# Performance work log

Measured on AMD Instinct MI355X. Metric: run time of the kernel, lower is better.

Reference implementation:

```python
import jax, jax.numpy as jnp
import numpy as np

HIDDEN = 1024
N_HEADS = 16
HEAD_DIM = HIDDEN // N_HEADS
WINDOW = 256
HALF_W = WINDOW // 2  # 128
GLOBAL_TOKENS = (0,)


def setup_inputs() -> dict:
    key = jax.random.key(0)
    ks = jax.random.split(key, 5)
    B, S = 1, 4096
    scale = 0.02
    return {
        "x": jax.random.normal(ks[0], (B, S, HIDDEN), dtype=jnp.float32),
        "Wq": jax.random.normal(ks[1], (HIDDEN, HIDDEN), dtype=jnp.float32) * scale,
        "Wk": jax.random.normal(ks[2], (HIDDEN, HIDDEN), dtype=jnp.float32) * scale,
        "Wv": jax.random.normal(ks[3], (HIDDEN, HIDDEN), dtype=jnp.float32) * scale,
        "Wo": jax.random.normal(ks[4], (HIDDEN, HIDDEN), dtype=jnp.float32) * scale,
    }


def _longformer_mask(seq_len: int) -> jnp.ndarray:
    # sliding window |i-j| <= half_w, plus full rows/cols for global tokens
    idx = jnp.arange(seq_len)
    mask = jnp.abs(idx[:, None] - idx[None, :]) <= HALF_W
    for g in GLOBAL_TOKENS:
        if 0 <= g < seq_len:
            mask = mask.at[g, :].set(True)
            mask = mask.at[:, g].set(True)
    return mask  # [S, S] bool


def reference(x, Wq, Wk, Wv, Wo):
    B, S, H = x.shape
    scale = HEAD_DIM ** -0.5
    # nn.Linear(bias=False): y = x @ W.T ; split heads -> [B, nH, S, hd]
    def proj(W):
        return jnp.einsum('bsh,oh->bso', x, W).reshape(B, S, N_HEADS, HEAD_DIM).transpose(0, 2, 1, 3)
    q, k, v = proj(Wq), proj(Wk), proj(Wv)
    scores = jnp.einsum('bnsd,bntd->bnst', q, k) * scale  # [B, nH, S, S]
    mask = _longformer_mask(S)
    scores = jnp.where(mask[None, None], scores, jnp.float32(-jnp.inf))
    attn = jax.nn.softmax(scores, axis=-1)
    out = jnp.einsum('bnst,bntd->bnsd', attn, v)  # [B, nH, S, hd]
    out = out.transpose(0, 2, 1, 3).reshape(B, S, H)
    return jnp.einsum('bsh,oh->bso', out, Wo)
```

## Files before the change

### kernel.cpp

```cpp
#include <hip/hip_runtime.h>
#include <hip/hip_bf16.h>
#include <stdint.h>

#define S_LEN 4096
#define HID   1024
#define NH    16
#define HD    64
#define HWIN  128

typedef __bf16 bf16x8 __attribute__((ext_vector_type(8)));
typedef float  f32x4  __attribute__((ext_vector_type(4)));
typedef unsigned short u16x8 __attribute__((ext_vector_type(8)));

typedef const __attribute__((address_space(1))) unsigned int* gas_ptr;
typedef __attribute__((address_space(3))) unsigned int* las_ptr;

__device__ __forceinline__ float bf2f(unsigned short u) {
  union { float f; uint32_t i; } w; w.i = ((uint32_t)u) << 16; return w.f;
}
__device__ __forceinline__ unsigned short f2bf(float f) {
  union { float f; uint32_t i; } w; w.f = f;
  uint32_t r = (w.i + 0x7FFFu + ((w.i >> 16) & 1u)) >> 16;
  return (unsigned short)r;
}

__device__ __forceinline__ void gld_lds16(const void* g, void* l) {
  __builtin_amdgcn_global_load_lds((gas_ptr)g, (las_ptr)l, 16, 0, 0);
}

__global__ __launch_bounds__(256) void convert_all(
    const float* __restrict__ x,
    const float* __restrict__ wq, const float* __restrict__ wk,
    const float* __restrict__ wv, const float* __restrict__ wo,
    unsigned short* __restrict__ xb,
    unsigned short* __restrict__ wqb, unsigned short* __restrict__ wkb,
    unsigned short* __restrict__ wvb, unsigned short* __restrict__ wob) {
  const int XF4 = (S_LEN * HID) / 4;
  const int WF4 = (HID * HID) / 4;
  int i = blockIdx.x * 256 + threadIdx.x;
#pragma unroll
  for (int it = 0; it < 4; it++, i += 524288) {
    const float* in; unsigned short* out; int off;
    if (i < XF4) { in = x; out = xb; off = i; }
    else {
      int j = i - XF4;
      int w = j >> 18;
      off = j & (WF4 - 1);
      switch (w) {
        case 0:  in = wq; out = wqb; break;
        case 1:  in = wk; out = wkb; break;
        case 2:  in = wv; out = wvb; break;
        default: in = wo; out = wob; break;
      }
    }
    float4 v = reinterpret_cast<const float4*>(in)[off];
    ushort4 o;
    o.x = f2bf(v.x); o.y = f2bf(v.y); o.z = f2bf(v.z); o.w = f2bf(v.w);
    reinterpret_cast<ushort4*>(out)[off] = o;
  }
}

__device__ __forceinline__ void gemm_body(const unsigned short* __restrict__ A,
                                          const unsigned short* __restrict__ B,
                                          unsigned short* __restrict__ Cb,
                                          float* __restrict__ Cf, int mode) {
  __shared__ __align__(16) unsigned short SM[2 * 128 * 64];
  unsigned short* As = SM;
  unsigned short* Bs = SM + 128 * 64;
  constexpr int K = HID;
  const int tid  = threadIdx.x;
  const int lane = tid & 63;
  const int wave = tid >> 6;
  const int wm = wave >> 1, wn = wave & 1;
  const int m0 = blockIdx.x * 128;
  const int n0 = blockIdx.y * 128;
  const int cl = lane & 15, g = lane >> 4;

  f32x4 acc[4][4];
#pragma unroll
  for (int i = 0; i < 4; i++)
#pragma unroll
    for (int j = 0; j < 4; j++) acc[i][j] = f32x4{0.f, 0.f, 0.f, 0.f};

  const unsigned short* Ap[4];
  const unsigned short* Bp[4];
  int ldso[4];
#pragma unroll
  for (int u = 0; u < 4; u++) {
    int s = tid + u * 256;
    int row = s >> 3, c16 = s & 7;
    int sc = ((c16 ^ (row & 7)) << 3);
    Ap[u] = A + (size_t)(m0 + row) * K + sc;
    Bp[u] = B + (size_t)(n0 + row) * K + sc;
    ldso[u] = s * 8;
  }

  for (int k0 = 0; k0 < K; k0 += 64) {
#pragma unroll
    for (int u = 0; u < 4; u++) {
      gld_lds16(Ap[u] + k0, &As[ldso[u]]);
      gld_lds16(Bp[u] + k0, &Bs[ldso[u]]);
    }
    __syncthreads();
#pragma unroll
    for (int kk = 0; kk < 2; kk++) {
      bf16x8 a[4], b[4];
#pragma unroll
      for (int mi = 0; mi < 4; mi++) {
        int row = wm * 64 + mi * 16 + cl;
        int c16 = (kk * 4 + g) ^ (row & 7);
        a[mi] = *reinterpret_cast<const bf16x8*>(&As[row * 64 + c16 * 8]);
      }
#pragma unroll
      for (int ni = 0; ni < 4; ni++) {
        int row = wn * 64 + ni * 16 + cl;
        int c16 = (kk * 4 + g) ^ (row & 7);
        b[ni] = *reinterpret_cast<const bf16x8*>(&Bs[row * 64 + c16 * 8]);
      }
#pragma unroll
      for (int mi = 0; mi < 4; mi++)
#pragma unroll
        for (int ni = 0; ni < 4; ni++)
          acc[mi][ni] = __builtin_amdgcn_mfma_f32_16x16x32_bf16(a[mi], b[ni], acc[mi][ni], 0, 0, 0);
    }
    __syncthreads();
  }

  const int rl = g * 4;
  if (mode == 1) {
#pragma unroll
    for (int mi = 0; mi < 4; mi++)
#pragma unroll
      for (int ni = 0; ni < 4; ni++) {
        int c = wn * 64 + ni * 16 + cl;
        int slot = (wm * 16 + mi * 4 + g) ^ ((c & 7) << 2);
        uint2 u;
        u.x = (uint32_t)f2bf(acc[mi][ni][0]) | ((uint32_t)f2bf(acc[mi][ni][1]) << 16);
        u.y = (uint32_t)f2bf(acc[mi][ni][2]) | ((uint32_t)f2bf(acc[mi][ni][3]) << 16);
        *reinterpret_cast<uint2*>(&SM[c * 128 + slot * 4]) = u;
      }
    __syncthreads();
    const int rgrp = tid & 15;
#pragma unroll
    for (int p = 0; p < 8; p++) {
      int c = p * 16 + (tid >> 4);
      int s0 = (2 * rgrp) ^ ((c & 7) << 2);
      int s1 = (2 * rgrp + 1) ^ ((c & 7) << 2);
      uint2 a2 = *reinterpret_cast<const uint2*>(&SM[c * 128 + s0 * 4]);
      uint2 b2 = *reinterpret_cast<const uint2*>(&SM[c * 128 + s1 * 4]);
      uint4 o{a2.x, a2.y, b2.x, b2.y};
      *reinterpret_cast<uint4*>(&Cb[(size_t)(n0 + c) * S_LEN + m0 + rgrp * 8]) = o;
    }
    return;
  }
#pragma unroll
  for (int mi = 0; mi < 4; mi++)
#pragma unroll
    for (int ni = 0; ni < 4; ni++)
#pragma unroll
      for (int i = 0; i < 4; i++) {
        int r = m0 + wm * 64 + mi * 16 + rl + i;
        int c = n0 + wn * 64 + ni * 16 + cl;
        float v = acc[mi][ni][i];
        if (mode == 2) Cf[(size_t)r * HID + c] = v;
        else           Cb[(size_t)r * HID + c] = f2bf(v);
      }
}

__global__ __launch_bounds__(256, 2) void gemm_qkv(
    const unsigned short* __restrict__ xb,
    const unsigned short* __restrict__ wqb, const unsigned short* __restrict__ wkb,
    const unsigned short* __restrict__ wvb,
    unsigned short* __restrict__ Qb, unsigned short* __restrict__ Kb,
    unsigned short* __restrict__ Vt) {
  const unsigned short* B = (blockIdx.z == 0) ? wqb : (blockIdx.z == 1) ? wkb : wvb;
  unsigned short* C       = (blockIdx.z == 0) ? Qb  : (blockIdx.z == 1) ? Kb  : Vt;
  int mode = (blockIdx.z == 2) ? 1 : 0;
  gemm_body(xb, B, C, nullptr, mode);
}

__global__ __launch_bounds__(256, 2) void gemm_proj(
    unsigned short* __restrict__ Ob, const unsigned short* __restrict__ wob,
    const float* __restrict__ mw, const float* __restrict__ lw,
    const float* __restrict__ ow, float* __restrict__ out) {
  if (blockIdx.x == 0) {
    const float LOG2E = 1.44269504f;
    for (int cc = threadIdx.x; cc < HID; cc += 256) {
      int h = cc >> 6, d = cc & 63;
      float m_g = -1e30f;
#pragma unroll
      for (int c = 0; c < 16; c++) m_g = fmaxf(m_g, mw[h * 16 + c]);
      float lsum = 0.f, osum = 0.f;
#pragma unroll
      for (int c = 0; c < 16; c++) {
        float w = exp2f((mw[h * 16 + c] - m_g) * LOG2E);
        lsum += lw[h * 16 + c] * w;
        osum += ow[(size_t)(h * 16 + c) * HD + d] * w;
      }
      Ob[cc] = f2bf(osum / lsum);
    }
    asm volatile("s_waitcnt vmcnt(0)" ::: "memory");
    __syncthreads();
  }
  gemm_body(Ob, wob, nullptr, out, 2);
}

__global__ __launch_bounds__(256) void attn_win(
    const unsigned short* __restrict__ Qb,
    const unsigned short* __restrict__ Kb,
    const unsigned short* __restrict__ Vt,
    unsigned short* __restrict__ Ob,
    float* __restrict__ mw, float* __restrict__ lw, float* __restrict__ ow) {
  const int tid  = threadIdx.x;
  const int lane = tid & 63;
  const int wave = tid >> 6;

  if (blockIdx.x >= 1024) {
    const int bid = blockIdx.x - 1024;
    const int c = bid & 15, h = bid >> 4;
    const int k = c * 256 + tid;
    __shared__ float qsh[HD];
    __shared__ float ps[256];
    __shared__ float redm[4], redl[4];
    __shared__ float red2[4][HD];
    const float LOG2E = 1.44269504f;

    if (tid < HD) qsh[tid] = bf2f(Qb[h * HD + tid]);
    __syncthreads();

    const unsigned short* kr = Kb + (size_t)k * HID + h * HD;
    float acc = 0.f;
#pragma unroll
    for (int v8 = 0; v8 < 8; v8++) {
      u16x8 kv = *reinterpret_cast<const u16x8*>(kr + v8 * 8);
#pragma unroll
      for (int j = 0; j < 8; j++) acc += qsh[v8 * 8 + j] * bf2f(kv[j]);
    }
    float s = acc * 0.125f;

    float m = s;
#pragma unroll
    for (int d = 1; d < 64; d <<= 1) m = fmaxf(m, __shfl_xor(m, d, 64));
    if (lane == 0) redm[wave] = m;
    __syncthreads();
    float m_c = fmaxf(fmaxf(redm[0], redm[1]), fmaxf(redm[2], redm[3]));

    float p = exp2f((s - m_c) * LOG2E);
    ps[tid] = p;
    float l = p;
#pragma unroll
    for (int d = 1; d < 64; d <<= 1) l += __shfl_xor(l, d, 64);
    if (lane == 0) redl[wave] = l;
    __syncthreads();
    float l_c = redl[0] + redl[1] + redl[2] + redl[3];

    const int d = tid & 63, grp = tid >> 6;
    const unsigned short* vrow = Vt + (size_t)(h * HD + d) * S_LEN + c * 256 + grp * 64;
    float a2 = 0.f;
#pragma unroll
    for (int v8 = 0; v8 < 8; v8++) {
      u16x8 vv = *reinterpret_cast<const u16x8*>(vrow + v8 * 8);
#pragma unroll
      for (int j = 0; j < 8; j++) a2 += ps[grp * 64 + v8 * 8 + j] * bf2f(vv[j]);
    }
    red2[grp][d] = a2;
    __syncthreads();
    if (tid < HD) {
      float o = red2[0][tid] + red2[1][tid] + red2[2][tid] + red2[3][tid];
      ow[(size_t)(h * 16 + c) * HD + tid] = o;
    }
    if (tid == 0) { mw[h * 16 + c] = m_c; lw[h * 16 + c] = l_c; }
    return;
  }

  __shared__ __align__(16) unsigned short Kl[2][64 * 64];
  __shared__ __align__(16) unsigned short Vl[2][64 * 64];
  __shared__ __align__(16) unsigned short Ps[4][16 * 64];
  const int L  = (blockIdx.x & 7) * 128 + (blockIdx.x >> 3);
  const int h  = L >> 6;
  const int q0 = (L & 63) * 64;
  const int qr   = q0 + wave * 16;
  const int cl = lane & 15, g = lane >> 4, rl = g * 4;
  const float SCL = 0.125f * 1.44269504f;

  int kw0 = q0 - 128; if (kw0 < 0) kw0 = 0;
  int kw1 = q0 + 192; if (kw1 > S_LEN) kw1 = S_LEN;
  const int nc = (kw1 - kw0) >> 6;

  const int s0 = tid, s1 = tid + 256;
  const int kr0 = s0 >> 3, kc0 = ((s0 & 7) ^ (kr0 & 7)) << 3;
  const int kr1 = s1 >> 3, kc1 = ((s1 & 7) ^ (kr1 & 7)) << 3;
  const unsigned short* Kbase = Kb + h * HD;
  const unsigned short* Vbase = Vt + (size_t)h * HD * S_LEN;

  auto stage = [&](int kb, int b) {
    gld_lds16(Kbase + (size_t)(kb + kr0) * HID + kc0, &Kl[b][s0 * 8]);
    gld_lds16(Kbase + (size_t)(kb + kr1) * HID + kc1, &Kl[b][s1 * 8]);
    gld_lds16(Vbase + (size_t)kr0 * S_LEN + kb + kc0, &Vl[b][s0 * 8]);
    gld_lds16(Vbase + (size_t)kr1 * S_LEN + kb + kc1, &Vl[b][s1 * 8]);
  };

  stage(kw0, 0);

  bf16x8 qf[2], k0f[2];
  {
    const unsigned short* qb = Qb + (size_t)(qr + cl) * HID + h * HD + g * 8;
    qf[0] = *reinterpret_cast<const bf16x8*>(qb);
    qf[1] = *reinterpret_cast<const bf16x8*>(qb + 32);
    const unsigned short* k0 = Kb + h * HD + g * 8;
    k0f[0] = *reinterpret_cast<const bf16x8*>(k0);
    k0f[1] = *reinterpret_cast<const bf16x8*>(k0 + 32);
  }
  float v0[4];
#pragma unroll
  for (int nt = 0; nt < 4; nt++)
    v0[nt] = bf2f(Vt[(size_t)(h * HD + nt * 16 + cl) * S_LEN]);

  float m_i[4] = {-1e30f, -1e30f, -1e30f, -1e30f};
  float l_i[4] = {0.f, 0.f, 0.f, 0.f};
  f32x4 oacc[4];
#pragma unroll
  for (int nt = 0; nt < 4; nt++) oacc[nt] = f32x4{0.f, 0.f, 0.f, 0.f};

  __syncthreads();

  for (int c = 0; c < nc; c++) {
    const int cur = c & 1;
    const int kb = kw0 + c * 64;
    if (c + 1 < nc) stage(kw0 + (c + 1) * 64, cur ^ 1);

    bf16x8 kf[4][2];
#pragma unroll
    for (int t = 0; t < 4; t++) {
      int R = t * 16 + cl;
      kf[t][0] = *reinterpret_cast<const bf16x8*>(&Kl[cur][R * 64 + ((g ^ (R & 7)) << 3)]);
      kf[t][1] = *reinterpret_cast<const bf16x8*>(&Kl[cur][R * 64 + (((g + 4) ^ (R & 7)) << 3)]);
    }
    f32x4 s4[4];
    __builtin_amdgcn_s_setprio(1);
#pragma unroll
    for (int t = 0; t < 4; t++) {
      s4[t] = f32x4{0.f, 0.f, 0.f, 0.f};
      s4[t] = __builtin_amdgcn_mfma_f32_16x16x32_bf16(qf[0], kf[t][0], s4[t], 0, 0, 0);
      s4[t] = __builtin_amdgcn_mfma_f32_16x16x32_bf16(qf[1], kf[t][1], s4[t], 0, 0, 0);
    }
    __builtin_amdgcn_s_setprio(0);

    float sv[4][4], tm[4];
    if (kb >= qr - 113 && kb <= qr + 65) {
#pragma unroll
      for (int i = 0; i < 4; i++) {
        tm[i] = -1e30f;
#pragma unroll
        for (int t = 0; t < 4; t++) {
          float v = s4[t][i] * SCL;
          sv[t][i] = v;
          tm[i] = fmaxf(tm[i], v);
        }
      }
    } else {
#pragma unroll
      for (int i = 0; i < 4; i++) {
        int row = qr + rl + i;
        tm[i] = -1e30f;
#pragma unroll
        for (int t = 0; t < 4; t++) {
          int col = kb + t * 16 + cl;
          int d = row - col;
          float v = (d <= HWIN && d >= -HWIN) ? s4[t][i] * SCL : -1e30f;
          sv[t][i] = v;
          tm[i] = fmaxf(tm[i], v);
        }
      }
    }
#pragma unroll
    for (int dd = 1; dd < 16; dd <<= 1)
#pragma unroll
      for (int i = 0; i < 4; i++) tm[i] = fmaxf(tm[i], __shfl_xor(tm[i], dd, 16));

    float p[4][4], ps[4];
#pragma unroll
    for (int i = 0; i < 4; i++) {
      float mnew = fmaxf(m_i[i], tm[i]);
      float fac  = exp2f(m_i[i] - mnew);
      m_i[i] = mnew;
      float sum = 0.f;
#pragma unroll
      for (int t = 0; t < 4; t++) { p[t][i] = exp2f(sv[t][i] - mnew); sum += p[t][i]; }
      ps[i] = sum;
      l_i[i] *= fac;
#pragma unroll
      for (int nt = 0; nt < 4; nt++) oacc[nt][i] *= fac;
    }
#pragma unroll
    for (int dd = 1; dd < 16; dd <<= 1)
#pragma unroll
      for (int i = 0; i < 4; i++) ps[i] += __shfl_xor(ps[i], dd, 16);
#pragma unroll
    for (int i = 0; i < 4; i++) l_i[i] += ps[i];

#pragma unroll
    for (int t = 0; t < 4; t++)
#pragma unroll
      for (int i = 0; i < 4; i++) {
        int row = rl + i;
        Ps[wave][row * 64 + ((t * 16 + cl) ^ ((row & 7) << 3))] = f2bf(p[t][i]);
      }
    bf16x8 pf[2];
    pf[0] = *reinterpret_cast<const bf16x8*>(&Ps[wave][cl * 64 + ((g * 8) ^ ((cl & 7) << 3))]);
    pf[1] = *reinterpret_cast<const bf16x8*>(&Ps[wave][cl * 64 + ((32 + g * 8) ^ ((cl & 7) << 3))]);

    __builtin_amdgcn_s_setprio(1);
#pragma unroll
    for (int nt = 0; nt < 4; nt++) {
      int row = nt * 16 + cl;
      bf16x8 vf0 = *reinterpret_cast<const bf16x8*>(&Vl[cur][row * 64 + ((g ^ (row & 7)) << 3)]);
      bf16x8 vf1 = *reinterpret_cast<const bf16x8*>(&Vl[cur][row * 64 + (((g + 4) ^ (row & 7)) << 3)]);
      oacc[nt] = __builtin_amdgcn_mfma_f32_16x16x32_bf16(pf[0], vf0, oacc[nt], 0, 0, 0);
      oacc[nt] = __builtin_amdgcn_mfma_f32_16x16x32_bf16(pf[1], vf1, oacc[nt], 0, 0, 0);
    }
    __builtin_amdgcn_s_setprio(0);

    __syncthreads();
  }

  float part = 0.f;
#pragma unroll
  for (int s = 0; s < 2; s++)
#pragma unroll
    for (int j = 0; j < 8; j++) part += (float)qf[s][j] * (float)k0f[s][j];
  part += __shfl_xor(part, 16);
  part += __shfl_xor(part, 32);
  float s0q = part * SCL;
#pragma unroll
  for (int i = 0; i < 4; i++) {
    float z0 = __shfl(s0q, rl + i, 16);
    int row = qr + rl + i;
    if (row > HWIN) {
      float mnew = fmaxf(m_i[i], z0);
      float fac  = exp2f(m_i[i] - mnew);
      float p0   = exp2f(z0 - mnew);
      l_i[i] = l_i[i] * fac + p0;
#pragma unroll
      for (int nt = 0; nt < 4; nt++)
        oacc[nt][i] = oacc[nt][i] * fac + p0 * v0[nt];
    }
  }

#pragma unroll
  for (int nt = 0; nt < 4; nt++)
#pragma unroll
    for (int i = 0; i < 4; i++)
      Ob[(size_t)(qr + rl + i) * HID + h * HD + nt * 16 + cl] = f2bf(oacc[nt][i] / l_i[i]);
}

extern "C" void kernel_launch(void* const* d_in, const int* in_sizes, int n_in,
                              void* d_out, int out_size, void* d_ws, size_t ws_size,
                              hipStream_t stream) {
  const float* x  = (const float*)d_in[0];
  const float* wq = (const float*)d_in[1];
  const float* wk = (const float*)d_in[2];
  const float* wv = (const float*)d_in[3];
  const float* wo = (const float*)d_in[4];
  float* out = (float*)d_out;
  char* ws = (char*)d_ws;
  const size_t MB = 1024ull * 1024ull;
  unsigned short* xb  = (unsigned short*)(ws + 0 * MB);
  unsigned short* wqb = (unsigned short*)(ws + 8 * MB);
  unsigned short* wkb = (unsigned short*)(ws + 10 * MB);
  unsigned short* wvb = (unsigned short*)(ws + 12 * MB);
  unsigned short* wob = (unsigned short*)(ws + 14 * MB);
  unsigned short* Qb  = (unsigned short*)(ws + 16 * MB);
  unsigned short* Kb  = (unsigned short*)(ws + 24 * MB);
  unsigned short* Vt  = (unsigned short*)(ws + 32 * MB);
  unsigned short* Ob  = (unsigned short*)(ws + 40 * MB);
  float* mw = (float*)(ws + 48 * MB);
  float* lw = (float*)(ws + 48 * MB + 4096);
  float* ow = (float*)(ws + 48 * MB + 8192);

  dim3 blk(256);
  convert_all<<<dim3(2048), blk, 0, stream>>>(
      x, wq, wk, wv, wo, xb, wqb, wkb, wvb, wob);
  gemm_qkv<<<dim3(S_LEN / 128, HID / 128, 3), blk, 0, stream>>>(
      xb, wqb, wkb, wvb, Qb, Kb, Vt);
  attn_win<<<dim3(1280), blk, 0, stream>>>(Qb, Kb, Vt, Ob, mw, lw, ow);
  gemm_proj<<<dim3(S_LEN / 128, HID / 128), blk, 0, stream>>>(
      Ob, wob, mw, lw, ow, out);
}
```

Before: 91.53 us.

## Triple-buffer GEMM K-loop with async LDS loads and single barrier

```diff
diff --git a/kernel.cpp b/kernel.cpp
--- a/kernel.cpp
+++ b/kernel.cpp
@@ -64,10 +64,9 @@
                                           const unsigned short* __restrict__ B,
                                           unsigned short* __restrict__ Cb,
                                           float* __restrict__ Cf, int mode) {
-  __shared__ __align__(16) unsigned short SM[2 * 128 * 64];
-  unsigned short* As = SM;
-  unsigned short* Bs = SM + 128 * 64;
+  __shared__ __align__(16) unsigned short SM[24576];
   constexpr int K = HID;
+  constexpr int NT = K / 32;
   const int tid  = threadIdx.x;
   const int lane = tid & 63;
   const int wave = tid >> 6;
@@ -82,48 +81,62 @@
 #pragma unroll
     for (int j = 0; j < 4; j++) acc[i][j] = f32x4{0.f, 0.f, 0.f, 0.f};
 
-  const unsigned short* Ap[4];
-  const unsigned short* Bp[4];
-  int ldso[4];
-#pragma unroll
-  for (int u = 0; u < 4; u++) {
-    int s = tid + u * 256;
-    int row = s >> 3, c16 = s & 7;
-    int sc = ((c16 ^ (row & 7)) << 3);
-    Ap[u] = A + (size_t)(m0 + row) * K + sc;
-    Bp[u] = B + (size_t)(n0 + row) * K + sc;
-    ldso[u] = s * 8;
-  }
-
-  for (int k0 = 0; k0 < K; k0 += 64) {
-#pragma unroll
-    for (int u = 0; u < 4; u++) {
-      gld_lds16(Ap[u] + k0, &As[ldso[u]]);
-      gld_lds16(Bp[u] + k0, &Bs[ldso[u]]);
-    }
-    __syncthreads();
-#pragma unroll
-    for (int kk = 0; kk < 2; kk++) {
-      bf16x8 a[4], b[4];
-#pragma unroll
-      for (int mi = 0; mi < 4; mi++) {
-        int row = wm * 64 + mi * 16 + cl;
-        int c16 = (kk * 4 + g) ^ (row & 7);
-        a[mi] = *reinterpret_cast<const bf16x8*>(&As[row * 64 + c16 * 8]);
-      }
-#pragma unroll
-      for (int ni = 0; ni < 4; ni++) {
-        int row = wn * 64 + ni * 16 + cl;
-        int c16 = (kk * 4 + g) ^ (row & 7);
-        b[ni] = *reinterpret_cast<const bf16x8*>(&Bs[row * 64 + c16 * 8]);
-      }
-#pragma unroll
-      for (int mi = 0; mi < 4; mi++)
-#pragma unroll
-        for (int ni = 0; ni < 4; ni++)
-          acc[mi][ni] = __builtin_amdgcn_mfma_f32_16x16x32_bf16(a[mi], b[ni], acc[mi][ni], 0, 0, 0);
-    }
-    __syncthreads();
+  const int s0 = tid, s1 = tid + 256;
+  const int r0 = s0 >> 2, c0 = ((s0 & 3) ^ ((r0 >> 1) & 3)) << 3;
+  const int r1 = s1 >> 2, c1 = ((s1 & 3) ^ ((r1 >> 1) & 3)) << 3;
+  const unsigned short* A0 = A + (size_t)(m0 + r0) * K + c0;
+  const unsigned short* A1 = A + (size_t)(m0 + r1) * K + c1;
+  const unsigned short* B0 = B + (size_t)(n0 + r0) * K + c0;
+  const unsigned short* B1 = B + (size_t)(n0 + r1) * K + c1;
+
+  auto stage = [&](int t, int b) {
+    const int k0 = t * 32;
+    gld_lds16(A0 + k0, &SM[b * 4096 + s0 * 8]);
+    gld_lds16(A1 + k0, &SM[b * 4096 + s1 * 8]);
+    gld_lds16(B0 + k0, &SM[12288 + b * 4096 + s0 * 8]);
+    gld_lds16(B1 + k0, &SM[12288 + b * 4096 + s1 * 8]);
+  };
+
+  stage(0, 0);
+  stage(1, 1);
+  asm volatile("s_waitcnt vmcnt(4)" ::: "memory");
+  __builtin_amdgcn_s_barrier();
+  __builtin_amdgcn_sched_barrier(0);
+
+  int cur = 0;
+  for (int t = 0; t < NT; ++t) {
+    int nn = cur + 2; if (nn >= 3) nn -= 3;
+    const bool more = (t + 2 < NT);
+    if (more) stage(t + 2, nn);
+
+    const unsigned short* Ac = &SM[cur * 4096];
+    const unsigned short* Bc = &SM[12288 + cur * 4096];
+    bf16x8 a[4], b[4];
+#pragma unroll
+    for (int mi = 0; mi < 4; mi++) {
+      int row = wm * 64 + mi * 16 + cl;
+      a[mi] = *reinterpret_cast<const bf16x8*>(
+          &Ac[row * 32 + ((g ^ ((row >> 1) & 3)) << 3)]);
+    }
+#pragma unroll
+    for (int ni = 0; ni < 4; ni++) {
+      int row = wn * 64 + ni * 16 + cl;
+      b[ni] = *reinterpret_cast<const bf16x8*>(
+          &Bc[row * 32 + ((g ^ ((row >> 1) & 3)) << 3)]);
+    }
+    __builtin_amdgcn_s_setprio(1);
+#pragma unroll
+    for (int mi = 0; mi < 4; mi++)
+#pragma unroll
+      for (int ni = 0; ni < 4; ni++)
+        acc[mi][ni] = __builtin_amdgcn_mfma_f32_16x16x32_bf16(a[mi], b[ni], acc[mi][ni], 0, 0, 0);
+    __builtin_amdgcn_s_setprio(0);
+
+    if (more) asm volatile("s_waitcnt vmcnt(4)" ::: "memory");
+    else      asm volatile("s_waitcnt vmcnt(0)" ::: "memory");
+    __builtin_amdgcn_s_barrier();
+    __builtin_amdgcn_sched_barrier(0);
+    cur = (cur == 2) ? 0 : cur + 1;
   }
 
   const int rl = g * 4;
@@ -144,10 +157,10 @@
 #pragma unroll
     for (int p = 0; p < 8; p++) {
       int c = p * 16 + (tid >> 4);
-      int s0 = (2 * rgrp) ^ ((c & 7) << 2);
-      int s1 = (2 * rgrp + 1) ^ ((c & 7) << 2);
-      uint2 a2 = *reinterpret_cast<const uint2*>(&SM[c * 128 + s0 * 4]);
-      uint2 b2 = *reinterpret_cast<const uint2*>(&SM[c * 128 + s1 * 4]);
+      int sa = (2 * rgrp) ^ ((c & 7) << 2);
+      int sb = (2 * rgrp + 1) ^ ((c & 7) << 2);
+      uint2 a2 = *reinterpret_cast<const uint2*>(&SM[c * 128 + sa * 4]);
+      uint2 b2 = *reinterpret_cast<const uint2*>(&SM[c * 128 + sb * 4]);
       uint4 o{a2.x, a2.y, b2.x, b2.y};
       *reinterpret_cast<uint4*>(&Cb[(size_t)(n0 + c) * S_LEN + m0 + rgrp * 8]) = o;
     }
```

Result: slower. 94.13 us (+2.8%).

## Process two 16-row query tiles per wave to reuse K/V chunks in attention

Applied to the files above, without the earlier changes.

```diff
diff --git a/kernel.cpp b/kernel.cpp
--- a/kernel.cpp
+++ b/kernel.cpp
@@ -144,10 +144,10 @@
 #pragma unroll
     for (int p = 0; p < 8; p++) {
       int c = p * 16 + (tid >> 4);
-      int s0 = (2 * rgrp) ^ ((c & 7) << 2);
-      int s1 = (2 * rgrp + 1) ^ ((c & 7) << 2);
-      uint2 a2 = *reinterpret_cast<const uint2*>(&SM[c * 128 + s0 * 4]);
-      uint2 b2 = *reinterpret_cast<const uint2*>(&SM[c * 128 + s1 * 4]);
+      int sa = (2 * rgrp) ^ ((c & 7) << 2);
+      int sb = (2 * rgrp + 1) ^ ((c & 7) << 2);
+      uint2 a2 = *reinterpret_cast<const uint2*>(&SM[c * 128 + sa * 4]);
+      uint2 b2 = *reinterpret_cast<const uint2*>(&SM[c * 128 + sb * 4]);
       uint4 o{a2.x, a2.y, b2.x, b2.y};
       *reinterpret_cast<uint4*>(&Cb[(size_t)(n0 + c) * S_LEN + m0 + rgrp * 8]) = o;
     }
@@ -215,8 +215,8 @@
   const int lane = tid & 63;
   const int wave = tid >> 6;
 
-  if (blockIdx.x >= 1024) {
-    const int bid = blockIdx.x - 1024;
+  if (blockIdx.x >= 512) {
+    const int bid = blockIdx.x - 512;
     const int c = bid & 15, h = bid >> 4;
     const int k = c * 256 + tid;
     __shared__ float qsh[HD];
@@ -276,15 +276,15 @@
   __shared__ __align__(16) unsigned short Kl[2][64 * 64];
   __shared__ __align__(16) unsigned short Vl[2][64 * 64];
   __shared__ __align__(16) unsigned short Ps[4][16 * 64];
-  const int L  = (blockIdx.x & 7) * 128 + (blockIdx.x >> 3);
-  const int h  = L >> 6;
-  const int q0 = (L & 63) * 64;
-  const int qr   = q0 + wave * 16;
+  const int L  = (blockIdx.x & 7) * 64 + (blockIdx.x >> 3);
+  const int h  = L >> 5;
+  const int q0 = (L & 31) * 128;
+  const int qr0 = q0 + wave * 32;
   const int cl = lane & 15, g = lane >> 4, rl = g * 4;
   const float SCL = 0.125f * 1.44269504f;
 
   int kw0 = q0 - 128; if (kw0 < 0) kw0 = 0;
-  int kw1 = q0 + 192; if (kw1 > S_LEN) kw1 = S_LEN;
+  int kw1 = q0 + 256; if (kw1 > S_LEN) kw1 = S_LEN;
   const int nc = (kw1 - kw0) >> 6;
 
   const int s0 = tid, s1 = tid + 256;
@@ -302,11 +302,14 @@
 
   stage(kw0, 0);
 
-  bf16x8 qf[2], k0f[2];
+  bf16x8 qf[2][2], k0f[2];
   {
-    const unsigned short* qb = Qb + (size_t)(qr + cl) * HID + h * HD + g * 8;
-    qf[0] = *reinterpret_cast<const bf16x8*>(qb);
-    qf[1] = *reinterpret_cast<const bf16x8*>(qb + 32);
+#pragma unroll
+    for (int qt = 0; qt < 2; qt++) {
+      const unsigned short* qb = Qb + (size_t)(qr0 + qt * 16 + cl) * HID + h * HD + g * 8;
+      qf[qt][0] = *reinterpret_cast<const bf16x8*>(qb);
+      qf[qt][1] = *reinterpret_cast<const bf16x8*>(qb + 32);
+    }
     const unsigned short* k0 = Kb + h * HD + g * 8;
     k0f[0] = *reinterpret_cast<const bf16x8*>(k0);
     k0f[1] = *reinterpret_cast<const bf16x8*>(k0 + 32);
@@ -316,11 +319,15 @@
   for (int nt = 0; nt < 4; nt++)
     v0[nt] = bf2f(Vt[(size_t)(h * HD + nt * 16 + cl) * S_LEN]);
 
-  float m_i[4] = {-1e30f, -1e30f, -1e30f, -1e30f};
-  float l_i[4] = {0.f, 0.f, 0.f, 0.f};
-  f32x4 oacc[4];
-#pragma unroll
-  for (int nt = 0; nt < 4; nt++) oacc[nt] = f32x4{0.f, 0.f, 0.f, 0.f};
+  float m_i[2][4], l_i[2][4];
+  f32x4 oacc[2][4];
+#pragma unroll
+  for (int qt = 0; qt < 2; qt++)
+#pragma unroll
+    for (int nt = 0; nt < 4; nt++) {
+      m_i[qt][nt] = -1e30f; l_i[qt][nt] = 0.f;
+      oacc[qt][nt] = f32x4{0.f, 0.f, 0.f, 0.f};
+    }
 
   __syncthreads();
 
@@ -336,122 +343,138 @@
       kf[t][0] = *reinterpret_cast<const bf16x8*>(&Kl[cur][R * 64 + ((g ^ (R & 7)) << 3)]);
       kf[t][1] = *reinterpret_cast<const bf16x8*>(&Kl[cur][R * 64 + (((g + 4) ^ (R & 7)) << 3)]);
     }
-    f32x4 s4[4];
+    f32x4 s4[2][4];
     __builtin_amdgcn_s_setprio(1);
 #pragma unroll
-    for (int t = 0; t < 4; t++) {
-      s4[t] = f32x4{0.f, 0.f, 0.f, 0.f};
-      s4[t] = __builtin_amdgcn_mfma_f32_16x16x32_bf16(qf[0], kf[t][0], s4[t], 0, 0, 0);
-      s4[t] = __builtin_amdgcn_mfma_f32_16x16x32_bf16(qf[1], kf[t][1], s4[t], 0, 0, 0);
-    }
+    for (int qt = 0; qt < 2; qt++)
+#pragma unroll
+      for (int t = 0; t < 4; t++) {
+        s4[qt][t] = f32x4{0.f, 0.f, 0.f, 0.f};
+        s4[qt][t] = __builtin_amdgcn_mfma_f32_16x16x32_bf16(qf[qt][0], kf[t][0], s4[qt][t], 0, 0, 0);
+        s4[qt][t] = __builtin_amdgcn_mfma_f32_16x16x32_bf16(qf[qt][1], kf[t][1], s4[qt][t], 0, 0, 0);
+      }
     __builtin_amdgcn_s_setprio(0);
 
-    float sv[4][4], tm[4];
-    if (kb >= qr - 113 && kb <= qr + 65) {
+    float p[2][4][4];
+#pragma unroll
+    for (int qt = 0; qt < 2; qt++) {
+      const int qr = qr0 + qt * 16;
+      float sv[4][4], tm[4];
+      if (kb >= qr - 113 && kb <= qr + 65) {
+#pragma unroll
+        for (int i = 0; i < 4; i++) {
+          tm[i] = -1e30f;
+#pragma unroll
+          for (int t = 0; t < 4; t++) {
+            float v = s4[qt][t][i] * SCL;
+            sv[t][i] = v;
+            tm[i] = fmaxf(tm[i], v);
+          }
+        }
+      } else {
+#pragma unroll
+        for (int i = 0; i < 4; i++) {
+          int row = qr + rl + i;
+          tm[i] = -1e30f;
+#pragma unroll
+          for (int t = 0; t < 4; t++) {
+            int col = kb + t * 16 + cl;
+            int d = row - col;
+            float v = (d <= HWIN && d >= -HWIN) ? s4[qt][t][i] * SCL : -1e30f;
+            sv[t][i] = v;
+            tm[i] = fmaxf(tm[i], v);
+          }
+        }
+      }
+#pragma unroll
+      for (int dd = 1; dd < 16; dd <<= 1)
+#pragma unroll
+        for (int i = 0; i < 4; i++) tm[i] = fmaxf(tm[i], __shfl_xor(tm[i], dd, 16));
+
+      float ps[4];
 #pragma unroll
       for (int i = 0; i < 4; i++) {
-        tm[i] = -1e30f;
-#pragma unroll
-        for (int t = 0; t < 4; t++) {
-          float v = s4[t][i] * SCL;
-          sv[t][i] = v;
-          tm[i] = fmaxf(tm[i], v);
-        }
-      }
-    } else {
-#pragma unroll
-      for (int i = 0; i < 4; i++) {
-        int row = qr + rl + i;
-        tm[i] = -1e30f;
-#pragma unroll
-        for (int t = 0; t < 4; t++) {
-          int col = kb + t * 16 + cl;
-          int d = row - col;
-          float v = (d <= HWIN && d >= -HWIN) ? s4[t][i] * SCL : -1e30f;
-          sv[t][i] = v;
-          tm[i] = fmaxf(tm[i], v);
-        }
-      }
-    }
-#pragma unroll
-    for (int dd = 1; dd < 16; dd <<= 1)
-#pragma unroll
-      for (int i = 0; i < 4; i++) tm[i] = fmaxf(tm[i], __shfl_xor(tm[i], dd, 16));
-
-    float p[4][4], ps[4];
-#pragma unroll
-    for (int i = 0; i < 4; i++) {
-      float mnew = fmaxf(m_i[i], tm[i]);
-      float fac  = exp2f(m_i[i] - mnew);
-      m_i[i] = mnew;
-      float sum = 0.f;
-#pragma unroll
-      for (int t = 0; t < 4; t++) { p[t][i] = exp2f(sv[t][i] - mnew); sum += p[t][i]; }
-      ps[i] = sum;
-      l_i[i] *= fac;
-#pragma unroll
-      for (int nt = 0; nt < 4; nt++) oacc[nt][i] *= fac;
-    }
-#pragma unroll
-    for (int dd = 1; dd < 16; dd <<= 1)
-#pragma unroll
-      for (int i = 0; i < 4; i++) ps[i] += __shfl_xor(ps[i], dd, 16);
-#pragma unroll
-    for (int i = 0; i < 4; i++) l_i[i] += ps[i];
-
-#pragma unroll
-    for (int t = 0; t < 4; t++)
-#pragma unroll
-      for (int i = 0; i < 4; i++) {
-        int row = rl + i;
-        Ps[wave][row * 64 + ((t * 16 + cl) ^ ((row & 7) << 3))] = f2bf(p[t][i]);
-      }
-    bf16x8 pf[2];
-    pf[0] = *reinterpret_cast<const bf16x8*>(&Ps[wave][cl * 64 + ((g * 8) ^ ((cl & 7) << 3))]);
-    pf[1] = *reinterpret_cast<const bf16x8*>(&Ps[wave][cl * 64 + ((32 + g * 8) ^ ((cl & 7) << 3))]);
-
-    __builtin_amdgcn_s_setprio(1);
+        float mnew = fmaxf(m_i[qt][i], tm[i]);
+        float fac  = exp2f(m_i[qt][i] - mnew);
+        m_i[qt][i] = mnew;
+        float sum = 0.f;
+#pragma unroll
+        for (int t = 0; t < 4; t++) { p[qt][t][i] = exp2f(sv[t][i] - mnew); sum += p[qt][t][i]; }
+        ps[i] = sum;
+        l_i[qt][i] *= fac;
+#pragma unroll
+        for (int nt = 0; nt < 4; nt++) oacc[qt][nt][i] *= fac;
+      }
+#pragma unroll
+      for (int dd = 1; dd < 16; dd <<= 1)
+#pragma unroll
+        for (int i = 0; i < 4; i++) ps[i] += __shfl_xor(ps[i], dd, 16);
+#pragma unroll
+      for (int i = 0; i < 4; i++) l_i[qt][i] += ps[i];
+    }
+
+    bf16x8 vf[4][2];
 #pragma unroll
     for (int nt = 0; nt < 4; nt++) {
       int row = nt * 16 + cl;
-      bf16x8 vf0 = *reinterpret_cast<const bf16x8*>(&Vl[cur][row * 64 + ((g ^ (row & 7)) << 3)]);
-      bf16x8 vf1 = *reinterpret_cast<const bf16x8*>(&Vl[cur][row * 64 + (((g + 4) ^ (row & 7)) << 3)]);
-      oacc[nt] = __builtin_amdgcn_mfma_f32_16x16x32_bf16(pf[0], vf0, oacc[nt], 0, 0, 0);
-      oacc[nt] = __builtin_amdgcn_mfma_f32_16x16x32_bf16(pf[1], vf1, oacc[nt], 0, 0, 0);
-    }
-    __builtin_amdgcn_s_setprio(0);
-
-    __syncthreads();
-  }
-
-  float part = 0.f;
-#pragma unroll
-  for (int s = 0; s < 2; s++)
-#pragma unroll
-    for (int j = 0; j < 8; j++) part += (float)qf[s][j] * (float)k0f[s][j];
-  part += __shfl_xor(part, 16);
-  part += __shfl_xor(part, 32);
-  float s0q = part * SCL;
-#pragma unroll
-  for (int i = 0; i < 4; i++) {
-    float z0 = __shfl(s0q, rl + i, 16);
-    int row = qr + rl + i;
-    if (row > HWIN) {
-      float mnew = fmaxf(m_i[i], z0);
-      float fac  = exp2f(m_i[i] - mnew);
-      float p0   = exp2f(z0 - mnew);
-      l_i[i] = l_i[i] * fac + p0;
-#pragma unroll
-      for (int nt = 0; nt < 4; nt++)
-        oacc[nt][i] = oacc[nt][i] * fac + p0 * v0[nt];
-    }
-  }
-
-#pragma unroll
-  for (int nt = 0; nt < 4; nt++)
-#pragma unroll
-    for (int i = 0; i < 4; i++)
-      Ob[(size_t)(qr + rl + i) * HID + h * HD + nt * 16 + cl] = f2bf(oacc[nt][i] / l_i[i]);
+      vf[nt][0] = *reinterpret_cast<const bf16x8*>(&Vl[cur][row * 64 + ((g ^ (row & 7)) << 3)]);
+      vf[nt][1] = *reinterpret_cast<const bf16x8*>(&Vl[cur][row * 64 + (((g + 4) ^ (row & 7)) << 3)]);
+    }
+#pragma unroll
+    for (int qt = 0; qt < 2; qt++) {
+#pragma unroll
+      for (int t = 0; t < 4; t++)
+#pragma unroll
+        for (int i = 0; i < 4; i++) {
+          int row = rl + i;
+          Ps[wave][row * 64 + ((t * 16 + cl) ^ ((row & 7) << 3))] = f2bf(p[qt][t][i]);
+        }
+      bf16x8 pf0 = *reinterpret_cast<const bf16x8*>(&Ps[wave][cl * 64 + ((g * 8) ^ ((cl & 7) << 3))]);
+      bf16x8 pf1 = *reinterpret_cast<const bf16x8*>(&Ps[wave][cl * 64 + ((32 + g * 8) ^ ((cl & 7) << 3))]);
+      __builtin_amdgcn_s_setprio(1);
+#pragma unroll
+      for (int nt = 0; nt < 4; nt++) {
+        oacc[qt][nt] = __builtin_amdgcn_mfma_f32_16x16x32_bf16(pf0, vf[nt][0], oacc[qt][nt], 0, 0, 0);
+        oacc[qt][nt] = __builtin_amdgcn_mfma_f32_16x16x32_bf16(pf1, vf[nt][1], oacc[qt][nt], 0, 0, 0);
+      }
+      __builtin_amdgcn_s_setprio(0);
+    }
+
+    __syncthreads();
+  }
+
+#pragma unroll
+  for (int qt = 0; qt < 2; qt++) {
+    float part = 0.f;
+#pragma unroll
+    for (int s = 0; s < 2; s++)
+#pragma unroll
+      for (int j = 0; j < 8; j++) part += (float)qf[qt][s][j] * (float)k0f[s][j];
+    part += __shfl_xor(part, 16);
+    part += __shfl_xor(part, 32);
+    float s0q = part * SCL;
+    const int qr = qr0 + qt * 16;
+#pragma unroll
+    for (int i = 0; i < 4; i++) {
+      float z0 = __shfl(s0q, rl + i, 16);
+      int row = qr + rl + i;
+      if (row > HWIN) {
+        float mnew = fmaxf(m_i[qt][i], z0);
+        float fac  = exp2f(m_i[qt][i] - mnew);
+        float p0   = exp2f(z0 - mnew);
+        l_i[qt][i] = l_i[qt][i] * fac + p0;
+#pragma unroll
+        for (int nt = 0; nt < 4; nt++)
+          oacc[qt][nt][i] = oacc[qt][nt][i] * fac + p0 * v0[nt];
+      }
+    }
+#pragma unroll
+    for (int nt = 0; nt < 4; nt++)
+#pragma unroll
+      for (int i = 0; i < 4; i++)
+        Ob[(size_t)(qr + rl + i) * HID + h * HD + nt * 16 + cl] =
+            f2bf(oacc[qt][nt][i] / l_i[qt][i]);
+  }
 }
 
 extern "C" void kernel_launch(void* const* d_in, const int* in_sizes, int n_in,
@@ -483,7 +506,7 @@
       x, wq, wk, wv, wo, xb, wqb, wkb, wvb, wob);
   gemm_qkv<<<dim3(S_LEN / 128, HID / 128, 3), blk, 0, stream>>>(
       xb, wqb, wkb, wvb, Qb, Kb, Vt);
-  attn_win<<<dim3(1280), blk, 0, stream>>>(Qb, Kb, Vt, Ob, mw, lw, ow);
+  attn_win<<<dim3(768), blk, 0, stream>>>(Qb, Kb, Vt, Ob, mw, lw, ow);
   gemm_proj<<<dim3(S_LEN / 128, HID / 128), blk, 0, stream>>>(
       Ob, wob, mw, lw, ow, out);
 }
```

Result: no change. 92.97 us (+1.6%).
